# Optimization experiments

Hardware: AMD Instinct MI355X
Metric: run time of the kernel (lower is better)

The kernel has to match this reference:

```python
import jax, jax.numpy as jnp
import numpy as np

B, C, H, W = 32, 512, 24, 8
C8 = C // 8  # PAM query/key channels


def setup_inputs() -> dict:
    key = jax.random.key(0)
    k0, k1, k2, k3, k4 = jax.random.split(key, 5)
    x = jax.random.normal(k0, (B, C, H, W), dtype=jnp.float32)
    Wq = jax.random.normal(k1, (C8, C), dtype=jnp.float32) * 0.02
    bq = jnp.zeros((C8,), dtype=jnp.float32)
    Wk = jax.random.normal(k2, (C8, C), dtype=jnp.float32) * 0.02
    bk = jnp.zeros((C8,), dtype=jnp.float32)
    return {"x": x, "Wq": Wq, "bq": bq, "Wk": Wk, "bk": bk}


def reference(x, Wq, bq, Wk, bk):
    b, c, h, w = x.shape
    hw = h * w
    xf = x.reshape(b, c, hw)  # [B, C, hw]

    # QAConv: einsum('gchw,pcyx->gpyxhw') with kernel == x, then view(B,-1,hw,hw).
    # With m=(h,w) of features and n=(y,x) of kernel this is 'gcm,pcn->gpnm'.
    score = jnp.einsum('gcm,pcn->gpnm', xf, xf)  # [B, B, hw, hw]
    kernel_max = score.max(axis=3)               # max over feature positions -> [B, B, hw]

    # PAM: 1x1 conv projections then bmm(q^T, k).
    q = jnp.einsum('qc,bcm->bqm', Wq, xf) + bq[None, :, None]  # [B, C8, hw]
    k = jnp.einsum('qc,bcm->bqm', Wk, xf) + bk[None, :, None]  # [B, C8, hw]
    energy = jnp.einsum('bqm,bqn->bmn', q, k)                  # [B, hw, hw]
    pos_max = energy.max(axis=2)[None]                         # [1, B, hw]

    return jnp.concatenate([kernel_max, pos_max], axis=0)  # [B+1, B, hw]
```

## Files before the change

### kernel.cpp

```cpp
#include <hip/hip_runtime.h>

typedef __bf16 bf16x8 __attribute__((ext_vector_type(8)));
typedef float f32x4 __attribute__((ext_vector_type(4)));
typedef unsigned short u16x8 __attribute__((ext_vector_type(8)));
typedef unsigned short u16x4 __attribute__((ext_vector_type(4)));

#define B_ 32
#define CC 512
#define HW 192
#define C8_ 64
#define NTRI 528
#define TILE_B 24576
#define SMEM_BYTES 152064

__device__ inline unsigned short f2bf(float f) {
    unsigned u = __float_as_uint(f);
    unsigned r = (u + 0x7FFFu + ((u >> 16) & 1u)) >> 16;
    return (unsigned short)r;
}

__device__ inline void gload16(const void* g, void* l) {
    __builtin_amdgcn_global_load_lds(
        (const __attribute__((address_space(1))) unsigned*)g,
        (__attribute__((address_space(3))) unsigned*)l,
        16, 0, 0);
}

__global__ void k_transpose(const float* __restrict__ x,
                            unsigned short* __restrict__ xt) {
    __shared__ unsigned short tile[64 * 64];
    int b = blockIdx.x / 3, mt = blockIdx.x % 3;
    int m0 = mt * 64, c0 = blockIdx.y * 64;
    int t = threadIdx.x;
    const float* xb = x + (size_t)b * CC * HW + (size_t)c0 * HW + m0;

    int mq = t & 15, cl0 = t >> 4;
    int sw = (mq & 7) << 3;
    #pragma unroll
    for (int rd = 0; rd < 4; ++rd) {
        int cl = rd * 16 + cl0;
        f32x4 v = *(const f32x4*)(xb + cl * HW + mq * 4);
        #pragma unroll
        for (int e = 0; e < 4; ++e)
            tile[(mq * 4 + e) * 64 + (cl ^ sw)] = f2bf(v[e]);
    }
    __syncthreads();
    unsigned short* xo = xt + ((size_t)b * HW + m0) * CC + c0;
    int kc = t & 7, mr0 = t >> 3;
    #pragma unroll
    for (int rd = 0; rd < 2; ++rd) {
        int mr = rd * 32 + mr0;
        u16x8 v = *(const u16x8*)&tile[mr * 64 + ((kc << 3) ^ (((mr >> 2) & 7) << 3))];
        *(u16x8*)(xo + (size_t)mr * CC + kc * 8) = v;
    }
}

__global__ void wcvt(const float* __restrict__ Wq, const float* __restrict__ Wk,
                     unsigned short* __restrict__ wqb, unsigned short* __restrict__ wkb) {
    const float* src = (blockIdx.x < 32) ? Wq : Wk;
    unsigned short* dst = (blockIdx.x < 32) ? wqb : wkb;
    int base = (blockIdx.x & 31) * 1024 + threadIdx.x * 4;
    f32x4 a = *(const f32x4*)(src + base);
    u16x4 o;
    #pragma unroll
    for (int e = 0; e < 4; ++e) o[e] = f2bf(a[e]);
    *(u16x4*)(dst + base) = o;
}

__global__ __launch_bounds__(256) void pam_qk(
        const unsigned short* __restrict__ xt,
        const unsigned short* __restrict__ wqb, const unsigned short* __restrict__ wkb,
        const float* __restrict__ bq, const float* __restrict__ bk,
        unsigned short* __restrict__ qo, unsigned short* __restrict__ ko) {
    int b = blockIdx.x, m0 = blockIdx.y * 48;
    int tid = threadIdx.x, w = tid >> 6, lane = tid & 63;
    int l15 = lane & 15, lq = lane >> 4;
    int qc = w * 16 + l15;

    f32x4 accq[3], acck[3];
    #pragma unroll
    for (int i = 0; i < 3; ++i) {
        accq[i] = (f32x4){0.f, 0.f, 0.f, 0.f};
        acck[i] = (f32x4){0.f, 0.f, 0.f, 0.f};
    }

    const unsigned short* xb = xt + ((size_t)b * HW + m0) * CC;
    const unsigned short* wqp = wqb + (size_t)qc * CC;
    const unsigned short* wkp = wkb + (size_t)qc * CC;

    for (int kt = 0; kt < 16; ++kt) {
        int ko8 = kt * 32 + lq * 8;
        bf16x8 wqf = *(const bf16x8*)(wqp + ko8);
        bf16x8 wkf = *(const bf16x8*)(wkp + ko8);
        bf16x8 af[3];
        #pragma unroll
        for (int i = 0; i < 3; ++i)
            af[i] = *(const bf16x8*)(xb + (i * 16 + l15) * CC + ko8);
        #pragma unroll
        for (int i = 0; i < 3; ++i) {
            accq[i] = __builtin_amdgcn_mfma_f32_16x16x32_bf16(af[i], wqf, accq[i], 0, 0, 0);
            acck[i] = __builtin_amdgcn_mfma_f32_16x16x32_bf16(af[i], wkf, acck[i], 0, 0, 0);
        }
    }

    float bqv = bq[qc], bkv = bk[qc];
    #pragma unroll
    for (int i = 0; i < 3; ++i) {
        #pragma unroll
        for (int r = 0; r < 4; ++r) {
            int m = m0 + i * 16 + lq * 4 + r;
            qo[((size_t)b * HW + m) * C8_ + qc] = f2bf(accq[i][r] + bqv);
            ko[((size_t)b * HW + m) * C8_ + qc] = f2bf(acck[i][r] + bkv);
        }
    }
}

__global__ __launch_bounds__(256) void pam_energy(
        const unsigned short* __restrict__ qo,
        const unsigned short* __restrict__ ko,
        float* __restrict__ out) {
    int b = blockIdx.x, m0 = blockIdx.y * 48;
    int tid = threadIdx.x, w = tid >> 6, lane = tid & 63;
    int l15 = lane & 15, lq = lane >> 4;
    int n0 = w * 48;

    f32x4 acc[3][3];
    #pragma unroll
    for (int i = 0; i < 3; ++i)
        #pragma unroll
        for (int j = 0; j < 3; ++j)
            acc[i][j] = (f32x4){0.f, 0.f, 0.f, 0.f};

    const unsigned short* qb = qo + ((size_t)b * HW + m0) * C8_;
    const unsigned short* kb = ko + ((size_t)b * HW + n0) * C8_;

    #pragma unroll
    for (int kt = 0; kt < 2; ++kt) {
        int ko8 = kt * 32 + lq * 8;
        bf16x8 af[3], bfr[3];
        #pragma unroll
        for (int i = 0; i < 3; ++i)
            af[i] = *(const bf16x8*)(qb + (i * 16 + l15) * C8_ + ko8);
        #pragma unroll
        for (int j = 0; j < 3; ++j)
            bfr[j] = *(const bf16x8*)(kb + (j * 16 + l15) * C8_ + ko8);
        #pragma unroll
        for (int i = 0; i < 3; ++i)
            #pragma unroll
            for (int j = 0; j < 3; ++j)
                acc[i][j] = __builtin_amdgcn_mfma_f32_16x16x32_bf16(af[i], bfr[j], acc[i][j], 0, 0, 0);
    }

    __shared__ float red[4][48];
    #pragma unroll
    for (int i = 0; i < 3; ++i) {
        float rm[4];
        #pragma unroll
        for (int r = 0; r < 4; ++r) rm[r] = -1e30f;
        #pragma unroll
        for (int j = 0; j < 3; ++j)
            #pragma unroll
            for (int r = 0; r < 4; ++r)
                rm[r] = fmaxf(rm[r], acc[i][j][r]);
        #pragma unroll
        for (int msk = 1; msk <= 8; msk <<= 1)
            #pragma unroll
            for (int r = 0; r < 4; ++r)
                rm[r] = fmaxf(rm[r], __shfl_xor(rm[r], msk));
        if (l15 == 0) {
            #pragma unroll
            for (int r = 0; r < 4; ++r)
                red[w][i * 16 + lq * 4 + r] = rm[r];
        }
    }
    __syncthreads();
    if (tid < 48) {
        float v = fmaxf(fmaxf(red[0][tid], red[1][tid]),
                        fmaxf(red[2][tid], red[3][tid]));
        out[((size_t)B_ * B_ + b) * HW + m0 + tid] = v;
    }
}

__global__ __launch_bounds__(512) void gram(const unsigned short* __restrict__ xt,
                                            float* __restrict__ out) {
    extern __shared__ char smem[];
    float* colbuf = (float*)(smem + 6 * TILE_B);
    float* rowbuf = (float*)(smem + 6 * TILE_B + 1536);

    int tid = threadIdx.x;
    int bid = (blockIdx.x & 7) * 66 + (blockIdx.x >> 3);
    int idx = bid, g = 0;
    while (idx >= B_ - g) { idx -= B_ - g; ++g; }
    int p = g + idx;

    const unsigned short* xg = xt + (size_t)g * HW * CC;
    const unsigned short* xp = xt + (size_t)p * HW * CC;

    int w = tid >> 6, lane = tid & 63;
    int wr = w >> 2, wc = w & 3;
    int l15 = lane & 15, lq = lane >> 4;

    int l8 = lane >> 3, s8 = lane & 7;
    const unsigned short* agp = xg + (size_t)(24 * w + l8) * CC + ((s8 ^ l8) << 3);
    const unsigned short* bgp = xp + (size_t)(24 * w + l8) * CC + ((s8 ^ l8) << 3);
    unsigned ldsw = (unsigned)(24 * w) * 128;

    unsigned aoff[6], boff[3];
    #pragma unroll
    for (int i = 0; i < 6; ++i) {
        int row = wr * 96 + i * 16 + l15;
        aoff[i] = row * 128 + ((unsigned)(lq ^ (row & 7)) << 4);
    }
    #pragma unroll
    for (int j = 0; j < 3; ++j) {
        int row = wc * 48 + j * 16 + l15;
        boff[j] = row * 128 + ((unsigned)(lq ^ (row & 7)) << 4);
    }

    f32x4 acc[6][3];
    #pragma unroll
    for (int i = 0; i < 6; ++i)
        #pragma unroll
        for (int j = 0; j < 3; ++j)
            acc[i][j] = (f32x4){0.f, 0.f, 0.f, 0.f};

    #define STAGE(buf, k0)                                                     \
        {                                                                      \
            char* ab = smem + (buf) * (2 * TILE_B) + ldsw;                     \
            char* bb = ab + TILE_B;                                            \
            _Pragma("unroll")                                                  \
            for (int ci = 0; ci < 3; ++ci) {                                   \
                gload16(agp + (k0) + ci * 8 * CC, ab + ci * 1024);             \
                gload16(bgp + (k0) + ci * 8 * CC, bb + ci * 1024);             \
            }                                                                  \
        }

    #define COMPUTE(buf)                                                       \
        {                                                                      \
            const char* Ab = smem + (buf) * (2 * TILE_B);                      \
            const char* Bb = Ab + TILE_B;                                      \
            _Pragma("unroll")                                                  \
            for (int kx = 0; kx < 128; kx += 64) {                             \
                bf16x8 af[6], bfr[3];                                          \
                _Pragma("unroll")                                              \
                for (int i = 0; i < 6; ++i)                                    \
                    af[i] = *(const bf16x8*)(Ab + (aoff[i] ^ kx));             \
                _Pragma("unroll")                                              \
                for (int j = 0; j < 3; ++j)                                    \
                    bfr[j] = *(const bf16x8*)(Bb + (boff[j] ^ kx));            \
                _Pragma("unroll")                                              \
                for (int i = 0; i < 6; ++i)                                    \
                    _Pragma("unroll")                                          \
                    for (int j = 0; j < 3; ++j)                                \
                        acc[i][j] = __builtin_amdgcn_mfma_f32_16x16x32_bf16(   \
                            af[i], bfr[j], acc[i][j], 0, 0, 0);                \
            }                                                                  \
        }

    #define WAIT6() asm volatile("s_waitcnt vmcnt(6)" ::: "memory")
    #define WAIT0() asm volatile("s_waitcnt vmcnt(0)" ::: "memory")
    #define BAR()   { __builtin_amdgcn_sched_barrier(0); __builtin_amdgcn_s_barrier(); }

    STAGE(0, 0);
    STAGE(1, 64);

    WAIT6(); BAR(); STAGE(2, 2 * 64); COMPUTE(0);
    WAIT6(); BAR(); STAGE(0, 3 * 64); COMPUTE(1);
    WAIT6(); BAR(); STAGE(1, 4 * 64); COMPUTE(2);
    WAIT6(); BAR(); STAGE(2, 5 * 64); COMPUTE(0);
    WAIT6(); BAR(); STAGE(0, 6 * 64); COMPUTE(1);
    WAIT6(); BAR(); STAGE(1, 7 * 64); COMPUTE(2);
    WAIT6(); BAR();                   COMPUTE(0);
    WAIT0(); BAR();                   COMPUTE(1);

    #pragma unroll
    for (int j = 0; j < 3; ++j) {
        float cm = -1e30f;
        #pragma unroll
        for (int i = 0; i < 6; ++i)
            #pragma unroll
            for (int r = 0; r < 4; ++r)
                cm = fmaxf(cm, acc[i][j][r]);
        cm = fmaxf(cm, __shfl_xor(cm, 16));
        cm = fmaxf(cm, __shfl_xor(cm, 32));
        if (lane < 16) colbuf[wr * HW + wc * 48 + j * 16 + l15] = cm;
    }
    #pragma unroll
    for (int i = 0; i < 6; ++i) {
        float rm[4];
        #pragma unroll
        for (int r = 0; r < 4; ++r) rm[r] = -1e30f;
        #pragma unroll
        for (int j = 0; j < 3; ++j)
            #pragma unroll
            for (int r = 0; r < 4; ++r)
                rm[r] = fmaxf(rm[r], acc[i][j][r]);
        #pragma unroll
        for (int msk = 1; msk <= 8; msk <<= 1)
            #pragma unroll
            for (int r = 0; r < 4; ++r)
                rm[r] = fmaxf(rm[r], __shfl_xor(rm[r], msk));
        if (l15 == 0) {
            #pragma unroll
            for (int r = 0; r < 4; ++r)
                rowbuf[wc * HW + wr * 96 + i * 16 + lq * 4 + r] = rm[r];
        }
    }
    __syncthreads();
    if (tid < HW) {
        float cmax = fmaxf(colbuf[tid], colbuf[HW + tid]);
        out[((size_t)g * B_ + p) * HW + tid] = cmax;
        float rmax = fmaxf(fmaxf(rowbuf[tid], rowbuf[HW + tid]),
                           fmaxf(rowbuf[2 * HW + tid], rowbuf[3 * HW + tid]));
        out[((size_t)p * B_ + g) * HW + tid] = rmax;
    }
}

extern "C" void kernel_launch(void* const* d_in, const int* in_sizes, int n_in,
                              void* d_out, int out_size, void* d_ws, size_t ws_size,
                              hipStream_t stream) {
    (void)in_sizes; (void)n_in; (void)out_size; (void)ws_size;
    const float* x  = (const float*)d_in[0];
    const float* Wq = (const float*)d_in[1];
    const float* bq = (const float*)d_in[2];
    const float* Wk = (const float*)d_in[3];
    const float* bk = (const float*)d_in[4];
    float* out = (float*)d_out;

    char* ws = (char*)d_ws;
    unsigned short* xt  = (unsigned short*)ws;
    unsigned short* wqb = (unsigned short*)(ws + 6291456);
    unsigned short* wkb = (unsigned short*)(ws + 6291456 + 65536);
    unsigned short* qbuf = (unsigned short*)(ws + 6291456 + 131072);
    unsigned short* kbuf = (unsigned short*)(ws + 6291456 + 131072 + 786432);

    hipFuncSetAttribute((const void*)gram,
                        hipFuncAttributeMaxDynamicSharedMemorySize, SMEM_BYTES);

    k_transpose<<<dim3(96, 8), dim3(256), 0, stream>>>(x, xt);
    wcvt<<<dim3(64), dim3(256), 0, stream>>>(Wq, Wk, wqb, wkb);
    pam_qk<<<dim3(32, 4), dim3(256), 0, stream>>>(xt, wqb, wkb, bq, bk, qbuf, kbuf);
    pam_energy<<<dim3(32, 4), dim3(256), 0, stream>>>(qbuf, kbuf, out);
    gram<<<dim3(NTRI), dim3(512), SMEM_BYTES, stream>>>(xt, out);
}
```

Baseline: 63.98 us.

## Split gram tiles in half, double-buffer, fuse prep and energy finalize kernels

Each pair's Gram tile is now split into two 96-row halves across twice as many blocks. That halves shared memory per block (triple to double buffering) and the accumulator count, so more blocks can be resident per CU. Column maxima from the two halves go to a workspace and are combined in a finalize pass fused into the PAM energy kernel. The transpose and weight-conversion kernels are merged into one launch, removing a kernel. The trade is re-reading the p-side data twice, an extra global round trip for partial maxima, and shallower prefetch with a full __syncthreads per k-step.

```diff
diff --git a/kernel.cpp b/kernel.cpp
--- a/kernel.cpp
+++ b/kernel.cpp
@@ -10,8 +10,9 @@
 #define HW 192
 #define C8_ 64
 #define NTRI 528
-#define TILE_B 24576
-#define SMEM_BYTES 152064
+#define NG2 1056
+#define BUF_B 36864
+#define SMEM_BYTES 73728
 
 __device__ inline unsigned short f2bf(float f) {
     unsigned u = __float_as_uint(f);
@@ -26,12 +27,26 @@
         16, 0, 0);
 }
 
-__global__ void k_transpose(const float* __restrict__ x,
-                            unsigned short* __restrict__ xt) {
+__global__ void prep(const float* __restrict__ x,
+                     const float* __restrict__ Wq, const float* __restrict__ Wk,
+                     unsigned short* __restrict__ xt,
+                     unsigned short* __restrict__ wqb, unsigned short* __restrict__ wkb) {
     __shared__ unsigned short tile[64 * 64];
+    int t = threadIdx.x;
+    if (blockIdx.x >= 96) {
+        int id = (blockIdx.x - 96) * 8 + blockIdx.y;
+        const float* src = (id < 32) ? Wq : Wk;
+        unsigned short* dst = (id < 32) ? wqb : wkb;
+        int base = (id & 31) * 1024 + t * 4;
+        f32x4 a = *(const f32x4*)(src + base);
+        u16x4 o;
+        #pragma unroll
+        for (int e = 0; e < 4; ++e) o[e] = f2bf(a[e]);
+        *(u16x4*)(dst + base) = o;
+        return;
+    }
     int b = blockIdx.x / 3, mt = blockIdx.x % 3;
     int m0 = mt * 64, c0 = blockIdx.y * 64;
-    int t = threadIdx.x;
     const float* xb = x + (size_t)b * CC * HW + (size_t)c0 * HW + m0;
 
     int mq = t & 15, cl0 = t >> 4;
@@ -53,18 +68,6 @@
         u16x8 v = *(const u16x8*)&tile[mr * 64 + ((kc << 3) ^ (((mr >> 2) & 7) << 3))];
         *(u16x8*)(xo + (size_t)mr * CC + kc * 8) = v;
     }
-}
-
-__global__ void wcvt(const float* __restrict__ Wq, const float* __restrict__ Wk,
-                     unsigned short* __restrict__ wqb, unsigned short* __restrict__ wkb) {
-    const float* src = (blockIdx.x < 32) ? Wq : Wk;
-    unsigned short* dst = (blockIdx.x < 32) ? wqb : wkb;
-    int base = (blockIdx.x & 31) * 1024 + threadIdx.x * 4;
-    f32x4 a = *(const f32x4*)(src + base);
-    u16x4 o;
-    #pragma unroll
-    for (int e = 0; e < 4; ++e) o[e] = f2bf(a[e]);
-    *(u16x4*)(dst + base) = o;
 }
 
 __global__ __launch_bounds__(256) void pam_qk(
@@ -115,12 +118,168 @@
     }
 }
 
-__global__ __launch_bounds__(256) void pam_energy(
+__global__ __launch_bounds__(512, 4) void gram2(const unsigned short* __restrict__ xt,
+                                                float* __restrict__ out,
+                                                float* __restrict__ ws2) {
+    extern __shared__ char smem[];
+
+    int tid = threadIdx.x;
+    int bid = (blockIdx.x & 7) * 132 + (blockIdx.x >> 3);
+    int pairid = bid >> 1, h = bid & 1;
+    int idx = pairid, g = 0;
+    while (idx >= B_ - g) { idx -= B_ - g; ++g; }
+    int p = g + idx;
+
+    const unsigned short* xga = xt + ((size_t)g * HW + 96 * h) * CC;
+    const unsigned short* xp  = xt + (size_t)p * HW * CC;
+
+    int w = tid >> 6, lane = tid & 63;
+    int wr = w >> 2, wc = w & 3;
+    int l15 = lane & 15, lq = lane >> 4;
+
+    const unsigned short* sp[5];
+    unsigned lo[5];
+    #pragma unroll
+    for (int ci = 0; ci < 5; ++ci) {
+        int R = (ci < 4) ? (w + 8 * ci) : (32 + w);
+        int q = R * 64 + lane;
+        if (ci == 4 && w >= 4) q = lane;
+        lo[ci] = (unsigned)q * 16;
+        if (q < 768) {
+            int r = q >> 3, s = q & 7;
+            sp[ci] = xga + r * CC + ((s ^ (r & 7)) << 3);
+        } else {
+            int q2 = q - 768, n = q2 >> 3, s = q2 & 7;
+            sp[ci] = xp + n * CC + ((s ^ (n & 7)) << 3);
+        }
+    }
+
+    unsigned aoff[3], boff[3];
+    #pragma unroll
+    for (int i = 0; i < 3; ++i) {
+        int row = wr * 48 + i * 16 + l15;
+        aoff[i] = (unsigned)row * 128 + ((unsigned)(lq ^ (row & 7)) << 4);
+    }
+    #pragma unroll
+    for (int j = 0; j < 3; ++j) {
+        int n = wc * 48 + j * 16 + l15;
+        boff[j] = 12288u + (unsigned)n * 128 + ((unsigned)(lq ^ (n & 7)) << 4);
+    }
+
+    f32x4 acc[3][3];
+    #pragma unroll
+    for (int i = 0; i < 3; ++i)
+        #pragma unroll
+        for (int j = 0; j < 3; ++j)
+            acc[i][j] = (f32x4){0.f, 0.f, 0.f, 0.f};
+
+    #define STG2(buf, kt)                                                      \
+        {                                                                      \
+            char* base = smem + (buf) * BUF_B;                                 \
+            int k0 = (kt) * 64;                                                \
+            gload16(sp[0] + k0, base + lo[0]);                                 \
+            gload16(sp[1] + k0, base + lo[1]);                                 \
+            gload16(sp[2] + k0, base + lo[2]);                                 \
+            gload16(sp[3] + k0, base + lo[3]);                                 \
+            if (w < 4) gload16(sp[4] + k0, base + lo[4]);                      \
+        }
+
+    #define CMP2(buf)                                                          \
+        {                                                                      \
+            const char* Bb = smem + (buf) * BUF_B;                             \
+            _Pragma("unroll")                                                  \
+            for (int kx = 0; kx < 128; kx += 64) {                             \
+                bf16x8 af[3], bfr[3];                                          \
+                _Pragma("unroll")                                              \
+                for (int i = 0; i < 3; ++i)                                    \
+                    af[i] = *(const bf16x8*)(Bb + (aoff[i] ^ kx));             \
+                _Pragma("unroll")                                              \
+                for (int j = 0; j < 3; ++j)                                    \
+                    bfr[j] = *(const bf16x8*)(Bb + (boff[j] ^ kx));            \
+                _Pragma("unroll")                                              \
+                for (int i = 0; i < 3; ++i)                                    \
+                    _Pragma("unroll")                                          \
+                    for (int j = 0; j < 3; ++j)                                \
+                        acc[i][j] = __builtin_amdgcn_mfma_f32_16x16x32_bf16(   \
+                            af[i], bfr[j], acc[i][j], 0, 0, 0);                \
+            }                                                                  \
+        }
+
+    STG2(0, 0);
+    __syncthreads();
+    for (int kt = 0; kt < 8; ++kt) {
+        int cur = kt & 1;
+        if (kt < 7) STG2(cur ^ 1, kt + 1);
+        CMP2(cur);
+        __syncthreads();
+    }
+
+    float* rowbuf = (float*)smem;
+    float* colbuf = (float*)(smem + 1536);
+
+    #pragma unroll
+    for (int i = 0; i < 3; ++i) {
+        float rm[4];
+        #pragma unroll
+        for (int r = 0; r < 4; ++r) rm[r] = -1e30f;
+        #pragma unroll
+        for (int j = 0; j < 3; ++j)
+            #pragma unroll
+            for (int r = 0; r < 4; ++r)
+                rm[r] = fmaxf(rm[r], acc[i][j][r]);
+        #pragma unroll
+        for (int msk = 1; msk <= 8; msk <<= 1)
+            #pragma unroll
+            for (int r = 0; r < 4; ++r)
+                rm[r] = fmaxf(rm[r], __shfl_xor(rm[r], msk));
+        if (l15 == 0) {
+            #pragma unroll
+            for (int r = 0; r < 4; ++r)
+                rowbuf[wc * 96 + wr * 48 + i * 16 + lq * 4 + r] = rm[r];
+        }
+    }
+    #pragma unroll
+    for (int j = 0; j < 3; ++j) {
+        float cm = -1e30f;
+        #pragma unroll
+        for (int i = 0; i < 3; ++i)
+            #pragma unroll
+            for (int r = 0; r < 4; ++r)
+                cm = fmaxf(cm, acc[i][j][r]);
+        cm = fmaxf(cm, __shfl_xor(cm, 16));
+        cm = fmaxf(cm, __shfl_xor(cm, 32));
+        if (lane < 16) colbuf[wr * HW + wc * 48 + j * 16 + l15] = cm;
+    }
+    __syncthreads();
+    if (tid < 96) {
+        float v = fmaxf(fmaxf(rowbuf[tid], rowbuf[96 + tid]),
+                        fmaxf(rowbuf[192 + tid], rowbuf[288 + tid]));
+        out[((size_t)p * B_ + g) * HW + 96 * h + tid] = v;
+    }
+    if (tid >= 128 && tid < 320) {
+        int n = tid - 128;
+        ws2[(size_t)pairid * 384 + h * 192 + n] = fmaxf(colbuf[n], colbuf[HW + n]);
+    }
+}
+
+__global__ __launch_bounds__(256) void energy_fin(
         const unsigned short* __restrict__ qo,
         const unsigned short* __restrict__ ko,
+        const float* __restrict__ ws2,
         float* __restrict__ out) {
-    int b = blockIdx.x, m0 = blockIdx.y * 48;
-    int tid = threadIdx.x, w = tid >> 6, lane = tid & 63;
+    int tid = threadIdx.x;
+    if (blockIdx.x >= 128) {
+        int pairid = blockIdx.x - 128;
+        int idx = pairid, g = 0;
+        while (idx >= B_ - g) { idx -= B_ - g; ++g; }
+        int p = g + idx;
+        if (tid < HW)
+            out[((size_t)g * B_ + p) * HW + tid] =
+                fmaxf(ws2[(size_t)pairid * 384 + tid], ws2[(size_t)pairid * 384 + 192 + tid]);
+        return;
+    }
+    int b = blockIdx.x >> 2, m0 = (blockIdx.x & 3) * 48;
+    int w = tid >> 6, lane = tid & 63;
     int l15 = lane & 15, lq = lane >> 4;
     int n0 = w * 48;
 
@@ -178,141 +337,6 @@
         float v = fmaxf(fmaxf(red[0][tid], red[1][tid]),
                         fmaxf(red[2][tid], red[3][tid]));
         out[((size_t)B_ * B_ + b) * HW + m0 + tid] = v;
-    }
-}
-
-__global__ __launch_bounds__(512) void gram(const unsigned short* __restrict__ xt,
-                                            float* __restrict__ out) {
-    extern __shared__ char smem[];
-    float* colbuf = (float*)(smem + 6 * TILE_B);
-    float* rowbuf = (float*)(smem + 6 * TILE_B + 1536);
-
-    int tid = threadIdx.x;
-    int bid = (blockIdx.x & 7) * 66 + (blockIdx.x >> 3);
-    int idx = bid, g = 0;
-    while (idx >= B_ - g) { idx -= B_ - g; ++g; }
-    int p = g + idx;
-
-    const unsigned short* xg = xt + (size_t)g * HW * CC;
-    const unsigned short* xp = xt + (size_t)p * HW * CC;
-
-    int w = tid >> 6, lane = tid & 63;
-    int wr = w >> 2, wc = w & 3;
-    int l15 = lane & 15, lq = lane >> 4;
-
-    int l8 = lane >> 3, s8 = lane & 7;
-    const unsigned short* agp = xg + (size_t)(24 * w + l8) * CC + ((s8 ^ l8) << 3);
-    const unsigned short* bgp = xp + (size_t)(24 * w + l8) * CC + ((s8 ^ l8) << 3);
-    unsigned ldsw = (unsigned)(24 * w) * 128;
-
-    unsigned aoff[6], boff[3];
-    #pragma unroll
-    for (int i = 0; i < 6; ++i) {
-        int row = wr * 96 + i * 16 + l15;
-        aoff[i] = row * 128 + ((unsigned)(lq ^ (row & 7)) << 4);
-    }
-    #pragma unroll
-    for (int j = 0; j < 3; ++j) {
-        int row = wc * 48 + j * 16 + l15;
-        boff[j] = row * 128 + ((unsigned)(lq ^ (row & 7)) << 4);
-    }
-
-    f32x4 acc[6][3];
-    #pragma unroll
-    for (int i = 0; i < 6; ++i)
-        #pragma unroll
-        for (int j = 0; j < 3; ++j)
-            acc[i][j] = (f32x4){0.f, 0.f, 0.f, 0.f};
-
-    #define STAGE(buf, k0)                                                     \
-        {                                                                      \
-            char* ab = smem + (buf) * (2 * TILE_B) + ldsw;                     \
-            char* bb = ab + TILE_B;                                            \
-            _Pragma("unroll")                                                  \
-            for (int ci = 0; ci < 3; ++ci) {                                   \
-                gload16(agp + (k0) + ci * 8 * CC, ab + ci * 1024);             \
-                gload16(bgp + (k0) + ci * 8 * CC, bb + ci * 1024);             \
-            }                                                                  \
-        }
-
-    #define COMPUTE(buf)                                                       \
-        {                                                                      \
-            const char* Ab = smem + (buf) * (2 * TILE_B);                      \
-            const char* Bb = Ab + TILE_B;                                      \
-            _Pragma("unroll")                                                  \
-            for (int kx = 0; kx < 128; kx += 64) {                             \
-                bf16x8 af[6], bfr[3];                                          \
-                _Pragma("unroll")                                              \
-                for (int i = 0; i < 6; ++i)                                    \
-                    af[i] = *(const bf16x8*)(Ab + (aoff[i] ^ kx));             \
-                _Pragma("unroll")                                              \
-                for (int j = 0; j < 3; ++j)                                    \
-                    bfr[j] = *(const bf16x8*)(Bb + (boff[j] ^ kx));            \
-                _Pragma("unroll")                                              \
-                for (int i = 0; i < 6; ++i)                                    \
-                    _Pragma("unroll")                                          \
-                    for (int j = 0; j < 3; ++j)                                \
-                        acc[i][j] = __builtin_amdgcn_mfma_f32_16x16x32_bf16(   \
-                            af[i], bfr[j], acc[i][j], 0, 0, 0);                \
-            }                                                                  \
-        }
-
-    #define WAIT6() asm volatile("s_waitcnt vmcnt(6)" ::: "memory")
-    #define WAIT0() asm volatile("s_waitcnt vmcnt(0)" ::: "memory")
-    #define BAR()   { __builtin_amdgcn_sched_barrier(0); __builtin_amdgcn_s_barrier(); }
-
-    STAGE(0, 0);
-    STAGE(1, 64);
-
-    WAIT6(); BAR(); STAGE(2, 2 * 64); COMPUTE(0);
-    WAIT6(); BAR(); STAGE(0, 3 * 64); COMPUTE(1);
-    WAIT6(); BAR(); STAGE(1, 4 * 64); COMPUTE(2);
-    WAIT6(); BAR(); STAGE(2, 5 * 64); COMPUTE(0);
-    WAIT6(); BAR(); STAGE(0, 6 * 64); COMPUTE(1);
-    WAIT6(); BAR(); STAGE(1, 7 * 64); COMPUTE(2);
-    WAIT6(); BAR();                   COMPUTE(0);
-    WAIT0(); BAR();                   COMPUTE(1);
-
-    #pragma unroll
-    for (int j = 0; j < 3; ++j) {
-        float cm = -1e30f;
-        #pragma unroll
-        for (int i = 0; i < 6; ++i)
-            #pragma unroll
-            for (int r = 0; r < 4; ++r)
-                cm = fmaxf(cm, acc[i][j][r]);
-        cm = fmaxf(cm, __shfl_xor(cm, 16));
-        cm = fmaxf(cm, __shfl_xor(cm, 32));
-        if (lane < 16) colbuf[wr * HW + wc * 48 + j * 16 + l15] = cm;
-    }
-    #pragma unroll
-    for (int i = 0; i < 6; ++i) {
-        float rm[4];
-        #pragma unroll
-        for (int r = 0; r < 4; ++r) rm[r] = -1e30f;
-        #pragma unroll
-        for (int j = 0; j < 3; ++j)
-            #pragma unroll
-            for (int r = 0; r < 4; ++r)
-                rm[r] = fmaxf(rm[r], acc[i][j][r]);
-        #pragma unroll
-        for (int msk = 1; msk <= 8; msk <<= 1)
-            #pragma unroll
-            for (int r = 0; r < 4; ++r)
-                rm[r] = fmaxf(rm[r], __shfl_xor(rm[r], msk));
-        if (l15 == 0) {
-            #pragma unroll
-            for (int r = 0; r < 4; ++r)
-                rowbuf[wc * HW + wr * 96 + i * 16 + lq * 4 + r] = rm[r];
-        }
-    }
-    __syncthreads();
-    if (tid < HW) {
-        float cmax = fmaxf(colbuf[tid], colbuf[HW + tid]);
-        out[((size_t)g * B_ + p) * HW + tid] = cmax;
-        float rmax = fmaxf(fmaxf(rowbuf[tid], rowbuf[HW + tid]),
-                           fmaxf(rowbuf[2 * HW + tid], rowbuf[3 * HW + tid]));
-        out[((size_t)p * B_ + g) * HW + tid] = rmax;
     }
 }
 
@@ -333,13 +357,13 @@
     unsigned short* wkb = (unsigned short*)(ws + 6291456 + 65536);
     unsigned short* qbuf = (unsigned short*)(ws + 6291456 + 131072);
     unsigned short* kbuf = (unsigned short*)(ws + 6291456 + 131072 + 786432);
-
-    hipFuncSetAttribute((const void*)gram,
+    float* ws2 = (float*)(ws + 6291456 + 131072 + 2 * 786432);
+
+    hipFuncSetAttribute((const void*)gram2,
                         hipFuncAttributeMaxDynamicSharedMemorySize, SMEM_BYTES);
 
-    k_transpose<<<dim3(96, 8), dim3(256), 0, stream>>>(x, xt);
-    wcvt<<<dim3(64), dim3(256), 0, stream>>>(Wq, Wk, wqb, wkb);
+    prep<<<dim3(104, 8), dim3(256), 0, stream>>>(x, Wq, Wk, xt, wqb, wkb);
     pam_qk<<<dim3(32, 4), dim3(256), 0, stream>>>(xt, wqb, wkb, bq, bk, qbuf, kbuf);
-    pam_energy<<<dim3(32, 4), dim3(256), 0, stream>>>(qbuf, kbuf, out);
-    gram<<<dim3(NTRI), dim3(512), SMEM_BYTES, stream>>>(xt, out);
-}
+    gram2<<<dim3(NG2), dim3(512), SMEM_BYTES, stream>>>(xt, out, ws2);
+    energy_fin<<<dim3(656), dim3(256), 0, stream>>>(qbuf, kbuf, ws2, out);
+}
```

Measured after the change: 56.38 us. -11.9%, faster.
